# Performance work log

Hardware: AMD Instinct MI355X
Metric: run time of the kernel (lower is better)

## Reference

```python
import jax, jax.numpy as jnp
import numpy as np


def setup_inputs() -> dict:
    key = jax.random.key(0)
    k_user, k_music, k_label, k_mem, k_w = jax.random.split(key, 5)
    B, H, N = 65536, 1024, 256  # batch, hidden (=2*hidden_size), memory slots
    user = jax.random.normal(k_user, (B, H), dtype=jnp.float32)
    music = jax.random.normal(k_music, (B, H), dtype=jnp.float32)
    memory = jax.random.normal(k_mem, (N, H), dtype=jnp.float32) * (1.0 / np.sqrt(H).astype(np.float32))
    W_out = jax.random.normal(k_w, (H, 2), dtype=jnp.float32) * (1.0 / np.sqrt(H).astype(np.float32))
    b_out = jnp.zeros((2,), dtype=jnp.float32)
    label = jax.random.randint(k_label, (B,), 0, 2, dtype=jnp.int64 if jax.config.jax_enable_x64 else jnp.int32)
    return {"user": user, "music": music, "memory": memory, "W_out": W_out, "b_out": b_out, "label": label}


def reference(user, music, memory, W_out, b_out, label):
    # s = user * music  (elementwise interaction)  [B, H]
    s = user * music
    # classification head: Linear(hidden, 2)
    out_result = s @ W_out + b_out  # [B, 2]
    # memory read: softmax(s @ memory^T) @ memory
    attn = jax.nn.softmax(s @ memory.T, axis=1)  # [B, N]
    rel = attn @ memory  # [B, H]
    # translational score: ||user + rel - music||_2 per row
    diff = user + rel - music
    score = jnp.sqrt(jnp.sum(diff * diff, axis=1))  # [B]
    mask = (2 * label - 1).astype(score.dtype)  # {-1, +1}
    loss = jnp.mean(mask * score)
    return loss, out_result
```

## Files before the change

### kernel.cpp

```cpp
#include <hip/hip_runtime.h>
#include <hip/hip_bf16.h>

typedef float ff4 __attribute__((ext_vector_type(4)));
typedef short s8v __attribute__((ext_vector_type(8)));
typedef unsigned int u4v __attribute__((ext_vector_type(4)));
typedef unsigned int u2v __attribute__((ext_vector_type(2)));

#define Hd 1024
#define Nn 256
#define RB 16
#define HSTR 520

__device__ __forceinline__ unsigned bf16r(float f) {
    unsigned u = __builtin_bit_cast(unsigned, f);
    return (u + 0x7FFFu + ((u >> 16) & 1u)) >> 16;
}

__device__ __forceinline__ unsigned cvtpk(float lo, float hi) {
    unsigned r;
    asm("v_cvt_pk_bf16_f32 %0, %1, %2" : "=v"(r) : "v"(lo), "v"(hi));
    return r;
}

__global__ void conv_mem_kernel(const float* __restrict__ mem, unsigned short* __restrict__ memB) {
    int g = blockIdx.x * 256 + threadIdx.x;
    int b = g & 3;
    int r = (g >> 2) & 255;
    int c = g >> 10;
    const float* src = mem + (size_t)r * Hd + c * 32 + b * 8;
    ff4 a0 = *(const ff4*)src;
    ff4 a1 = *(const ff4*)(src + 4);
    u4v v;
    v[0] = bf16r(a0[0]) | (bf16r(a0[1]) << 16);
    v[1] = bf16r(a0[2]) | (bf16r(a0[3]) << 16);
    v[2] = bf16r(a1[0]) | (bf16r(a1[1]) << 16);
    v[3] = bf16r(a1[2]) | (bf16r(a1[3]) << 16);
    *(u4v*)(memB + (size_t)c * 8192 + (size_t)r * 32 + b * 8) = v;
}

__global__ void conv_w_kernel(const float* __restrict__ Wout, unsigned short* __restrict__ Wbf) {
    int t = threadIdx.x;
    int c = t >> 7;
    int h0 = (t & 127) * 8;
    u4v v;
#pragma unroll
    for (int j = 0; j < 4; ++j) {
        unsigned lo = bf16r(Wout[(h0 + 2 * j) * 2 + c]);
        unsigned hi = bf16r(Wout[(h0 + 2 * j + 1) * 2 + c]);
        v[j] = lo | (hi << 16);
    }
    *(u4v*)(Wbf + (size_t)c * Hd + h0) = v;
}

__global__ __launch_bounds__(256) void gram_kernel(const float* __restrict__ mem,
                                                   unsigned short* __restrict__ Gcm) {
    __shared__ float LA[32][132];
    __shared__ float LB[32][132];
    const int t = threadIdx.x;
    const int bi = blockIdx.x >> 3, bj = blockIdx.x & 7;
    const int j = t & 31, i0 = t >> 5;
    float acc0 = 0.f, acc1 = 0.f, acc2 = 0.f, acc3 = 0.f;
    for (int kc = 0; kc < Hd; kc += 128) {
        __syncthreads();
#pragma unroll
        for (int q = 0; q < 4; ++q) {
            int c = t + q * 256;
            int r = c >> 5, fc = (c & 31) << 2;
            *(ff4*)&LA[r][fc] = *(const ff4*)(mem + (size_t)(bi * 32 + r) * Hd + kc + fc);
            *(ff4*)&LB[r][fc] = *(const ff4*)(mem + (size_t)(bj * 32 + r) * Hd + kc + fc);
        }
        __syncthreads();
#pragma unroll 4
        for (int kk = 0; kk < 128; kk += 4) {
            ff4 b = *(const ff4*)&LB[j][kk];
            ff4 a0 = *(const ff4*)&LA[i0][kk];
            ff4 a1 = *(const ff4*)&LA[i0 + 8][kk];
            ff4 a2 = *(const ff4*)&LA[i0 + 16][kk];
            ff4 a3 = *(const ff4*)&LA[i0 + 24][kk];
            acc0 += a0[0]*b[0] + a0[1]*b[1] + a0[2]*b[2] + a0[3]*b[3];
            acc1 += a1[0]*b[0] + a1[1]*b[1] + a1[2]*b[2] + a1[3]*b[3];
            acc2 += a2[0]*b[0] + a2[1]*b[1] + a2[2]*b[2] + a2[3]*b[3];
            acc3 += a3[0]*b[0] + a3[1]*b[1] + a3[2]*b[2] + a3[3]*b[3];
        }
    }
    const size_t base = (size_t)bj * 8192 + (size_t)j;
    Gcm[base + (size_t)(bi * 32 + i0 +  0) * 32] = (unsigned short)bf16r(acc0);
    Gcm[base + (size_t)(bi * 32 + i0 +  8) * 32] = (unsigned short)bf16r(acc1);
    Gcm[base + (size_t)(bi * 32 + i0 + 16) * 32] = (unsigned short)bf16r(acc2);
    Gcm[base + (size_t)(bi * 32 + i0 + 24) * 32] = (unsigned short)bf16r(acc3);
}

__global__ __launch_bounds__(256, 3) void fused_kernel(
    const float* __restrict__ user, const float* __restrict__ music,
    const float* __restrict__ bout, const int* __restrict__ label,
    const unsigned short* __restrict__ memB,
    const unsigned short* __restrict__ Wbf,
    const unsigned short* __restrict__ Gcm,
    float* __restrict__ out, float* __restrict__ partials)
{
    __shared__ __align__(16) unsigned short sS[RB * HSTR];
    __shared__ __align__(16) unsigned short sD[RB * HSTR];
    __shared__ float fMax[64], fSum[64], fCross[64], fQuad[64], fAux[16];
    unsigned short* sAttn = sS;

    const int t = threadIdx.x;
    const int w = t >> 6;
    const int l = t & 63;
    const int la = l & 15, lb = l >> 4;
    const int row0 = blockIdx.x * RB;

    const int srow = t >> 4;
    const int scol = t & 15;
    const float* uRow = user  + (size_t)(row0 + srow) * Hd + scol * 4;
    const float* mRow = music + (size_t)(row0 + srow) * Hd + scol * 4;

    const unsigned short* mbase = memB + w * 2048 + la * 32 + lb * 8;
    const unsigned short* wrowB = Wbf + (size_t)(la < 2 ? la : 1) * Hd + lb * 8;
    const unsigned short* gbase = Gcm + w * 2048 + la * 32 + lb * 8;
    const int aoff = la * HSTR + lb * 8;

    ff4 accL[4], accD[4];
#pragma unroll
    for (int i = 0; i < 4; ++i) { accL[i] = (ff4)0.0f; accD[i] = (ff4)0.0f; }
    ff4 accH = (ff4)0.0f;
    float sd2 = 0.f;

#pragma unroll
    for (int hh = 0; hh < 2; ++hh) {
#pragma unroll
        for (int i = 0; i < 8; ++i) {
            const int off = hh * 512 + 64 * i;
            ff4 uv = *(const ff4*)(uRow + off);
            ff4 mv = *(const ff4*)(mRow + off);
            float s0 = uv[0]*mv[0], s1 = uv[1]*mv[1], s2 = uv[2]*mv[2], s3 = uv[3]*mv[3];
            float d0 = uv[0]-mv[0], d1 = uv[1]-mv[1], d2 = uv[2]-mv[2], d3 = uv[3]-mv[3];
            sd2 = fmaf(d0,d0,sd2); sd2 = fmaf(d1,d1,sd2);
            sd2 = fmaf(d2,d2,sd2); sd2 = fmaf(d3,d3,sd2);
            u2v vs, vd;
            vs[0] = cvtpk(s0, s1); vs[1] = cvtpk(s2, s3);
            vd[0] = cvtpk(d0, d1); vd[1] = cvtpk(d2, d3);
            *(u2v*)(sS + srow * HSTR + scol * 4 + 64 * i) = vs;
            *(u2v*)(sD + srow * HSTR + scol * 4 + 64 * i) = vd;
        }
        __syncthreads();

        {
            const int c0 = hh * 16;
            s8v bMa[4], bMb[4], bWa, bWb, aSa, aSb, aDa, aDb;
#pragma unroll
            for (int nt = 0; nt < 4; ++nt)
                bMa[nt] = *(const s8v*)(mbase + (size_t)c0 * 8192 + nt * 512);
            bWa = *(const s8v*)(wrowB + c0 * 32);
            aSa = *(const s8v*)(sS + aoff);
            aDa = *(const s8v*)(sD + aoff);
#pragma unroll
            for (int kk = 0; kk < 16; kk += 2) {
                const int k1 = (kk + 1) & 15;
#pragma unroll
                for (int nt = 0; nt < 4; ++nt)
                    bMb[nt] = *(const s8v*)(mbase + (size_t)(c0 + k1) * 8192 + nt * 512);
                bWb = *(const s8v*)(wrowB + (c0 + k1) * 32);
                aSb = *(const s8v*)(sS + aoff + k1 * 32);
                aDb = *(const s8v*)(sD + aoff + k1 * 32);
#pragma unroll
                for (int nt = 0; nt < 4; ++nt) {
                    accL[nt] = __builtin_amdgcn_mfma_f32_16x16x32_bf16(aSa, bMa[nt], accL[nt], 0, 0, 0);
                    accD[nt] = __builtin_amdgcn_mfma_f32_16x16x32_bf16(aDa, bMa[nt], accD[nt], 0, 0, 0);
                }
                accH = __builtin_amdgcn_mfma_f32_16x16x32_bf16(aSa, bWa, accH, 0, 0, 0);
                const int k2 = (kk + 2) & 15;
#pragma unroll
                for (int nt = 0; nt < 4; ++nt)
                    bMa[nt] = *(const s8v*)(mbase + (size_t)(c0 + k2) * 8192 + nt * 512);
                bWa = *(const s8v*)(wrowB + (c0 + k2) * 32);
                aSa = *(const s8v*)(sS + aoff + k2 * 32);
                aDa = *(const s8v*)(sD + aoff + k2 * 32);
#pragma unroll
                for (int nt = 0; nt < 4; ++nt) {
                    accL[nt] = __builtin_amdgcn_mfma_f32_16x16x32_bf16(aSb, bMb[nt], accL[nt], 0, 0, 0);
                    accD[nt] = __builtin_amdgcn_mfma_f32_16x16x32_bf16(aDb, bMb[nt], accD[nt], 0, 0, 0);
                }
                accH = __builtin_amdgcn_mfma_f32_16x16x32_bf16(aSb, bWb, accH, 0, 0, 0);
            }
        }
        __syncthreads();
    }

    if (w == 0 && la < 2) {
#pragma unroll
        for (int j = 0; j < 4; ++j) {
            int gr = row0 + lb * 4 + j;
            out[1 + gr * 2 + la] = accH[j] + bout[la];
        }
    }

    sd2 += __shfl_xor(sd2, 1);
    sd2 += __shfl_xor(sd2, 2);
    sd2 += __shfl_xor(sd2, 4);
    sd2 += __shfl_xor(sd2, 8);
    if ((l & 15) == 0) fAux[w * 4 + (l >> 4)] = sd2;

    ff4 mx = accL[0];
#pragma unroll
    for (int nt = 1; nt < 4; ++nt) {
        mx[0] = fmaxf(mx[0], accL[nt][0]); mx[1] = fmaxf(mx[1], accL[nt][1]);
        mx[2] = fmaxf(mx[2], accL[nt][2]); mx[3] = fmaxf(mx[3], accL[nt][3]);
    }
#pragma unroll
    for (int s = 1; s < 16; s <<= 1) {
        mx[0] = fmaxf(mx[0], __shfl_xor(mx[0], s));
        mx[1] = fmaxf(mx[1], __shfl_xor(mx[1], s));
        mx[2] = fmaxf(mx[2], __shfl_xor(mx[2], s));
        mx[3] = fmaxf(mx[3], __shfl_xor(mx[3], s));
    }
    ff4 sm = (ff4)0.0f;
#pragma unroll
    for (int nt = 0; nt < 4; ++nt) {
        sm[0] += __expf(accL[nt][0] - mx[0]); sm[1] += __expf(accL[nt][1] - mx[1]);
        sm[2] += __expf(accL[nt][2] - mx[2]); sm[3] += __expf(accL[nt][3] - mx[3]);
    }
#pragma unroll
    for (int s = 1; s < 16; s <<= 1) {
        sm[0] += __shfl_xor(sm[0], s); sm[1] += __shfl_xor(sm[1], s);
        sm[2] += __shfl_xor(sm[2], s); sm[3] += __shfl_xor(sm[3], s);
    }
    if (la < 4) {
        const int r = lb * 4 + la;
        float mv = (la == 0) ? mx[0] : (la == 1) ? mx[1] : (la == 2) ? mx[2] : mx[3];
        float sv = (la == 0) ? sm[0] : (la == 1) ? sm[1] : (la == 2) ? sm[2] : sm[3];
        fMax[w * 16 + r] = mv;
        fSum[w * 16 + r] = sv;
    }
    __syncthreads();

    ff4 Mr, Dinv;
#pragma unroll
    for (int j = 0; j < 4; ++j) {
        const int r = lb * 4 + j;
        float m0 = fMax[r], m1 = fMax[16 + r], m2 = fMax[32 + r], m3 = fMax[48 + r];
        float M = fmaxf(fmaxf(m0, m1), fmaxf(m2, m3));
        float den = fSum[r] * __expf(m0 - M) + fSum[16 + r] * __expf(m1 - M)
                  + fSum[32 + r] * __expf(m2 - M) + fSum[48 + r] * __expf(m3 - M);
        Mr[j] = M; Dinv[j] = 1.0f / den;
    }
    ff4 cross = (ff4)0.0f;
#pragma unroll
    for (int nt = 0; nt < 4; ++nt) {
        accL[nt][0] = __expf(accL[nt][0] - Mr[0]) * Dinv[0];
        accL[nt][1] = __expf(accL[nt][1] - Mr[1]) * Dinv[1];
        accL[nt][2] = __expf(accL[nt][2] - Mr[2]) * Dinv[2];
        accL[nt][3] = __expf(accL[nt][3] - Mr[3]) * Dinv[3];
        cross[0] = fmaf(accL[nt][0], accD[nt][0], cross[0]);
        cross[1] = fmaf(accL[nt][1], accD[nt][1], cross[1]);
        cross[2] = fmaf(accL[nt][2], accD[nt][2], cross[2]);
        cross[3] = fmaf(accL[nt][3], accD[nt][3], cross[3]);
    }
#pragma unroll
    for (int s = 1; s < 16; s <<= 1) {
        cross[0] += __shfl_xor(cross[0], s); cross[1] += __shfl_xor(cross[1], s);
        cross[2] += __shfl_xor(cross[2], s); cross[3] += __shfl_xor(cross[3], s);
    }
    if (la < 4) {
        const int r = lb * 4 + la;
        float cv = (la == 0) ? cross[0] : (la == 1) ? cross[1] : (la == 2) ? cross[2] : cross[3];
        fCross[w * 16 + r] = cv;
    }
    {
        const int rb = lb << 2;
#pragma unroll
        for (int nt = 0; nt < 4; ++nt) {
            const int cc = w * 64 + nt * 16 + la;
            sAttn[(rb + 0) * 264 + cc] = (unsigned short)bf16r(accL[nt][0]);
            sAttn[(rb + 1) * 264 + cc] = (unsigned short)bf16r(accL[nt][1]);
            sAttn[(rb + 2) * 264 + cc] = (unsigned short)bf16r(accL[nt][2]);
            sAttn[(rb + 3) * 264 + cc] = (unsigned short)bf16r(accL[nt][3]);
        }
    }
    __syncthreads();

    ff4 accG[4];
#pragma unroll
    for (int i = 0; i < 4; ++i) accG[i] = (ff4)0.0f;
#pragma unroll
    for (int ks = 0; ks < 8; ++ks) {
        s8v aA = *(const s8v*)(sAttn + la * 264 + ks * 32 + lb * 8);
        const unsigned short* gp = gbase + (size_t)ks * 8192;
#pragma unroll
        for (int nt = 0; nt < 4; ++nt) {
            s8v bG = *(const s8v*)(gp + nt * 512);
            accG[nt] = __builtin_amdgcn_mfma_f32_16x16x32_bf16(aA, bG, accG[nt], 0, 0, 0);
        }
    }
    ff4 quad = (ff4)0.0f;
#pragma unroll
    for (int nt = 0; nt < 4; ++nt) {
        quad[0] = fmaf(accL[nt][0], accG[nt][0], quad[0]);
        quad[1] = fmaf(accL[nt][1], accG[nt][1], quad[1]);
        quad[2] = fmaf(accL[nt][2], accG[nt][2], quad[2]);
        quad[3] = fmaf(accL[nt][3], accG[nt][3], quad[3]);
    }
#pragma unroll
    for (int s = 1; s < 16; s <<= 1) {
        quad[0] += __shfl_xor(quad[0], s); quad[1] += __shfl_xor(quad[1], s);
        quad[2] += __shfl_xor(quad[2], s); quad[3] += __shfl_xor(quad[3], s);
    }
    if (la < 4) {
        const int r = lb * 4 + la;
        float qv = (la == 0) ? quad[0] : (la == 1) ? quad[1] : (la == 2) ? quad[2] : quad[3];
        fQuad[w * 16 + r] = qv;
    }
    __syncthreads();

    float val = 0.f;
    if (w == 0 && l < 16) {
        float cr  = fCross[l] + fCross[16 + l] + fCross[32 + l] + fCross[48 + l];
        float qd  = fQuad[l] + fQuad[16 + l] + fQuad[32 + l] + fQuad[48 + l];
        float s2 = fAux[l] + 2.0f * cr + qd;
        float sc = sqrtf(fmaxf(s2, 0.0f));
        val = (float)(2 * label[row0 + l] - 1) * sc;
    }
#pragma unroll
    for (int s = 1; s < 64; s <<= 1) val += __shfl_xor(val, s);
    if (t == 0) partials[blockIdx.x] = val;
}

__global__ void finalize_kernel(const float* __restrict__ partials, float* __restrict__ out,
                                int np, float invB) {
    const int t = threadIdx.x;
    float v = 0.f;
    for (int i = t; i < np; i += 256) v += partials[i];
#pragma unroll
    for (int s = 1; s < 64; s <<= 1) v += __shfl_xor(v, s);
    __shared__ float ws4[4];
    if ((t & 63) == 0) ws4[t >> 6] = v;
    __syncthreads();
    if (t == 0) out[0] = (ws4[0] + ws4[1] + ws4[2] + ws4[3]) * invB;
}

extern "C" void kernel_launch(void* const* d_in, const int* in_sizes, int n_in,
                              void* d_out, int out_size, void* d_ws, size_t ws_size,
                              hipStream_t stream) {
    const float* user  = (const float*)d_in[0];
    const float* music = (const float*)d_in[1];
    const float* mem   = (const float*)d_in[2];
    const float* Wout  = (const float*)d_in[3];
    const float* bout  = (const float*)d_in[4];
    const int*   label = (const int*)d_in[5];
    const int Bn   = in_sizes[0] / Hd;
    const int nblk = Bn / RB;

    unsigned short* memB = (unsigned short*)d_ws;
    unsigned short* Wbf  = (unsigned short*)((char*)d_ws + 524288);
    unsigned short* Gcm  = (unsigned short*)((char*)d_ws + 524288 + 4096);
    float* partials      = (float*)((char*)d_ws + 524288 + 4096 + 131072);

    conv_mem_kernel<<<128, 256, 0, stream>>>(mem, memB);
    conv_w_kernel<<<1, 256, 0, stream>>>(Wout, Wbf);
    gram_kernel<<<64, 256, 0, stream>>>(mem, Gcm);
    fused_kernel<<<nblk, 256, 0, stream>>>(user, music, bout, label, memB, Wbf, Gcm,
                                           (float*)d_out, partials);
    finalize_kernel<<<1, 256, 0, stream>>>(partials, (float*)d_out, nblk, 1.0f / (float)Bn);
}
```

Measured before the change: 269.3 us.

## Warp-specialize fused kernel into producer and MFMA consumer waves with double-buffered LDS

The block grows to 512 threads. Four producer waves load user and music, form the product and difference, and write them as bf16 into one of two small LDS slots, each holding a 128-column chunk. Four consumer waves run the MFMA logits and head products on the other slot, so global loads overlap with matrix work. This replaces the earlier two-phase fill-then-compute loop but adds eight barrier rounds and a larger block, which may cost occupancy and add synchronization overhead.

```diff
diff --git a/kernel.cpp b/kernel.cpp
--- a/kernel.cpp
+++ b/kernel.cpp
@@ -9,7 +9,8 @@
 #define Hd 1024
 #define Nn 256
 #define RB 16
-#define HSTR 520
+#define QSTR 136
+#define QSLOT 2176
 
 __device__ __forceinline__ unsigned bf16r(float f) {
     unsigned u = __builtin_bit_cast(unsigned, f);
@@ -90,7 +91,7 @@
     Gcm[base + (size_t)(bi * 32 + i0 + 24) * 32] = (unsigned short)bf16r(acc3);
 }
 
-__global__ __launch_bounds__(256, 3) void fused_kernel(
+__global__ __launch_bounds__(512, 4) void fused_kernel(
     const float* __restrict__ user, const float* __restrict__ music,
     const float* __restrict__ bout, const int* __restrict__ label,
     const unsigned short* __restrict__ memB,
@@ -98,8 +99,8 @@
     const unsigned short* __restrict__ Gcm,
     float* __restrict__ out, float* __restrict__ partials)
 {
-    __shared__ __align__(16) unsigned short sS[RB * HSTR];
-    __shared__ __align__(16) unsigned short sD[RB * HSTR];
+    __shared__ __align__(16) unsigned short sS[2 * QSLOT];
+    __shared__ __align__(16) unsigned short sD[2 * QSLOT];
     __shared__ float fMax[64], fSum[64], fCross[64], fQuad[64], fAux[16];
     unsigned short* sAttn = sS;
 
@@ -108,164 +109,152 @@
     const int l = t & 63;
     const int la = l & 15, lb = l >> 4;
     const int row0 = blockIdx.x * RB;
-
-    const int srow = t >> 4;
-    const int scol = t & 15;
-    const float* uRow = user  + (size_t)(row0 + srow) * Hd + scol * 4;
-    const float* mRow = music + (size_t)(row0 + srow) * Hd + scol * 4;
+    const bool isProd = (w >= 4);
+
+    const int pw = w - 4;
+    const int prow = pw * 4 + (l >> 4);
+    const int pcol = (l & 15) * 4;
+    const float* uP = user  + (size_t)(row0 + prow) * Hd + pcol;
+    const float* mP = music + (size_t)(row0 + prow) * Hd + pcol;
+    float sd2 = 0.f;
 
     const unsigned short* mbase = memB + w * 2048 + la * 32 + lb * 8;
     const unsigned short* wrowB = Wbf + (size_t)(la < 2 ? la : 1) * Hd + lb * 8;
     const unsigned short* gbase = Gcm + w * 2048 + la * 32 + lb * 8;
-    const int aoff = la * HSTR + lb * 8;
 
     ff4 accL[4], accD[4];
 #pragma unroll
     for (int i = 0; i < 4; ++i) { accL[i] = (ff4)0.0f; accD[i] = (ff4)0.0f; }
     ff4 accH = (ff4)0.0f;
-    float sd2 = 0.f;
-
-#pragma unroll
-    for (int hh = 0; hh < 2; ++hh) {
-#pragma unroll
-        for (int i = 0; i < 8; ++i) {
-            const int off = hh * 512 + 64 * i;
-            ff4 uv = *(const ff4*)(uRow + off);
-            ff4 mv = *(const ff4*)(mRow + off);
-            float s0 = uv[0]*mv[0], s1 = uv[1]*mv[1], s2 = uv[2]*mv[2], s3 = uv[3]*mv[3];
-            float d0 = uv[0]-mv[0], d1 = uv[1]-mv[1], d2 = uv[2]-mv[2], d3 = uv[3]-mv[3];
-            sd2 = fmaf(d0,d0,sd2); sd2 = fmaf(d1,d1,sd2);
-            sd2 = fmaf(d2,d2,sd2); sd2 = fmaf(d3,d3,sd2);
-            u2v vs, vd;
-            vs[0] = cvtpk(s0, s1); vs[1] = cvtpk(s2, s3);
-            vd[0] = cvtpk(d0, d1); vd[1] = cvtpk(d2, d3);
-            *(u2v*)(sS + srow * HSTR + scol * 4 + 64 * i) = vs;
-            *(u2v*)(sD + srow * HSTR + scol * 4 + 64 * i) = vd;
+
+#define FILL(QQ, SLOT)                                                          \
+    {                                                                           \
+        _Pragma("unroll")                                                       \
+        for (int i = 0; i < 2; ++i) {                                           \
+            const int off = (QQ) * 128 + i * 64;                                \
+            ff4 uv = *(const ff4*)(uP + off);                                   \
+            ff4 mv = *(const ff4*)(mP + off);                                   \
+            float s0 = uv[0]*mv[0], s1 = uv[1]*mv[1], s2 = uv[2]*mv[2], s3 = uv[3]*mv[3]; \
+            float d0 = uv[0]-mv[0], d1 = uv[1]-mv[1], d2 = uv[2]-mv[2], d3 = uv[3]-mv[3]; \
+            sd2 = fmaf(d0,d0,sd2); sd2 = fmaf(d1,d1,sd2);                       \
+            sd2 = fmaf(d2,d2,sd2); sd2 = fmaf(d3,d3,sd2);                       \
+            u2v vs, vd;                                                         \
+            vs[0] = cvtpk(s0, s1); vs[1] = cvtpk(s2, s3);                       \
+            vd[0] = cvtpk(d0, d1); vd[1] = cvtpk(d2, d3);                       \
+            *(u2v*)(sS + (SLOT) * QSLOT + prow * QSTR + i * 64 + pcol) = vs;    \
+            *(u2v*)(sD + (SLOT) * QSLOT + prow * QSTR + i * 64 + pcol) = vd;    \
+        }                                                                       \
+    }
+
+    if (isProd) FILL(0, 0)
+    __syncthreads();
+
+    for (int q = 0; q < 8; ++q) {
+        if (isProd) {
+            if (q < 7) FILL(q + 1, (q + 1) & 1)
+        } else {
+            const int s = q & 1;
+#pragma unroll
+            for (int kk = 0; kk < 4; ++kk) {
+                const int c = q * 4 + kk;
+                const unsigned short* mp = mbase + (size_t)c * 8192;
+                s8v aS = *(const s8v*)(sS + s * QSLOT + la * QSTR + kk * 32 + lb * 8);
+                s8v aD = *(const s8v*)(sD + s * QSLOT + la * QSTR + kk * 32 + lb * 8);
+                s8v bW = *(const s8v*)(wrowB + c * 32);
+#pragma unroll
+                for (int nt = 0; nt < 4; ++nt) {
+                    s8v bM = *(const s8v*)(mp + nt * 512);
+                    accL[nt] = __builtin_amdgcn_mfma_f32_16x16x32_bf16(aS, bM, accL[nt], 0, 0, 0);
+                    accD[nt] = __builtin_amdgcn_mfma_f32_16x16x32_bf16(aD, bM, accD[nt], 0, 0, 0);
+                }
+                accH = __builtin_amdgcn_mfma_f32_16x16x32_bf16(aS, bW, accH, 0, 0, 0);
+            }
         }
         __syncthreads();
-
-        {
-            const int c0 = hh * 16;
-            s8v bMa[4], bMb[4], bWa, bWb, aSa, aSb, aDa, aDb;
-#pragma unroll
-            for (int nt = 0; nt < 4; ++nt)
-                bMa[nt] = *(const s8v*)(mbase + (size_t)c0 * 8192 + nt * 512);
-            bWa = *(const s8v*)(wrowB + c0 * 32);
-            aSa = *(const s8v*)(sS + aoff);
-            aDa = *(const s8v*)(sD + aoff);
-#pragma unroll
-            for (int kk = 0; kk < 16; kk += 2) {
-                const int k1 = (kk + 1) & 15;
-#pragma unroll
-                for (int nt = 0; nt < 4; ++nt)
-                    bMb[nt] = *(const s8v*)(mbase + (size_t)(c0 + k1) * 8192 + nt * 512);
-                bWb = *(const s8v*)(wrowB + (c0 + k1) * 32);
-                aSb = *(const s8v*)(sS + aoff + k1 * 32);
-                aDb = *(const s8v*)(sD + aoff + k1 * 32);
-#pragma unroll
-                for (int nt = 0; nt < 4; ++nt) {
-                    accL[nt] = __builtin_amdgcn_mfma_f32_16x16x32_bf16(aSa, bMa[nt], accL[nt], 0, 0, 0);
-                    accD[nt] = __builtin_amdgcn_mfma_f32_16x16x32_bf16(aDa, bMa[nt], accD[nt], 0, 0, 0);
-                }
-                accH = __builtin_amdgcn_mfma_f32_16x16x32_bf16(aSa, bWa, accH, 0, 0, 0);
-                const int k2 = (kk + 2) & 15;
-#pragma unroll
-                for (int nt = 0; nt < 4; ++nt)
-                    bMa[nt] = *(const s8v*)(mbase + (size_t)(c0 + k2) * 8192 + nt * 512);
-                bWa = *(const s8v*)(wrowB + (c0 + k2) * 32);
-                aSa = *(const s8v*)(sS + aoff + k2 * 32);
-                aDa = *(const s8v*)(sD + aoff + k2 * 32);
-#pragma unroll
-                for (int nt = 0; nt < 4; ++nt) {
-                    accL[nt] = __builtin_amdgcn_mfma_f32_16x16x32_bf16(aSb, bMb[nt], accL[nt], 0, 0, 0);
-                    accD[nt] = __builtin_amdgcn_mfma_f32_16x16x32_bf16(aDb, bMb[nt], accD[nt], 0, 0, 0);
-                }
-                accH = __builtin_amdgcn_mfma_f32_16x16x32_bf16(aSb, bWb, accH, 0, 0, 0);
+    }
+#undef FILL
+
+    if (isProd) {
+        sd2 += __shfl_xor(sd2, 1);
+        sd2 += __shfl_xor(sd2, 2);
+        sd2 += __shfl_xor(sd2, 4);
+        sd2 += __shfl_xor(sd2, 8);
+        if ((l & 15) == 0) fAux[prow] = sd2;
+    }
+    if (!isProd) {
+        if (w == 0 && la < 2) {
+#pragma unroll
+            for (int j = 0; j < 4; ++j) {
+                int gr = row0 + lb * 4 + j;
+                out[1 + gr * 2 + la] = accH[j] + bout[la];
             }
         }
-        __syncthreads();
-    }
-
-    if (w == 0 && la < 2) {
+        ff4 mx = accL[0];
+#pragma unroll
+        for (int nt = 1; nt < 4; ++nt) {
+            mx[0] = fmaxf(mx[0], accL[nt][0]); mx[1] = fmaxf(mx[1], accL[nt][1]);
+            mx[2] = fmaxf(mx[2], accL[nt][2]); mx[3] = fmaxf(mx[3], accL[nt][3]);
+        }
+#pragma unroll
+        for (int s = 1; s < 16; s <<= 1) {
+            mx[0] = fmaxf(mx[0], __shfl_xor(mx[0], s));
+            mx[1] = fmaxf(mx[1], __shfl_xor(mx[1], s));
+            mx[2] = fmaxf(mx[2], __shfl_xor(mx[2], s));
+            mx[3] = fmaxf(mx[3], __shfl_xor(mx[3], s));
+        }
+        ff4 sm = (ff4)0.0f;
+#pragma unroll
+        for (int nt = 0; nt < 4; ++nt) {
+            sm[0] += __expf(accL[nt][0] - mx[0]); sm[1] += __expf(accL[nt][1] - mx[1]);
+            sm[2] += __expf(accL[nt][2] - mx[2]); sm[3] += __expf(accL[nt][3] - mx[3]);
+        }
+#pragma unroll
+        for (int s = 1; s < 16; s <<= 1) {
+            sm[0] += __shfl_xor(sm[0], s); sm[1] += __shfl_xor(sm[1], s);
+            sm[2] += __shfl_xor(sm[2], s); sm[3] += __shfl_xor(sm[3], s);
+        }
+        if (la < 4) {
+            const int r = lb * 4 + la;
+            float mv = (la == 0) ? mx[0] : (la == 1) ? mx[1] : (la == 2) ? mx[2] : mx[3];
+            float sv = (la == 0) ? sm[0] : (la == 1) ? sm[1] : (la == 2) ? sm[2] : sm[3];
+            fMax[w * 16 + r] = mv;
+            fSum[w * 16 + r] = sv;
+        }
+    }
+    __syncthreads();
+
+    ff4 Mr, Dinv, cross = (ff4)0.0f;
+    if (!isProd) {
 #pragma unroll
         for (int j = 0; j < 4; ++j) {
-            int gr = row0 + lb * 4 + j;
-            out[1 + gr * 2 + la] = accH[j] + bout[la];
-        }
-    }
-
-    sd2 += __shfl_xor(sd2, 1);
-    sd2 += __shfl_xor(sd2, 2);
-    sd2 += __shfl_xor(sd2, 4);
-    sd2 += __shfl_xor(sd2, 8);
-    if ((l & 15) == 0) fAux[w * 4 + (l >> 4)] = sd2;
-
-    ff4 mx = accL[0];
-#pragma unroll
-    for (int nt = 1; nt < 4; ++nt) {
-        mx[0] = fmaxf(mx[0], accL[nt][0]); mx[1] = fmaxf(mx[1], accL[nt][1]);
-        mx[2] = fmaxf(mx[2], accL[nt][2]); mx[3] = fmaxf(mx[3], accL[nt][3]);
-    }
-#pragma unroll
-    for (int s = 1; s < 16; s <<= 1) {
-        mx[0] = fmaxf(mx[0], __shfl_xor(mx[0], s));
-        mx[1] = fmaxf(mx[1], __shfl_xor(mx[1], s));
-        mx[2] = fmaxf(mx[2], __shfl_xor(mx[2], s));
-        mx[3] = fmaxf(mx[3], __shfl_xor(mx[3], s));
-    }
-    ff4 sm = (ff4)0.0f;
-#pragma unroll
-    for (int nt = 0; nt < 4; ++nt) {
-        sm[0] += __expf(accL[nt][0] - mx[0]); sm[1] += __expf(accL[nt][1] - mx[1]);
-        sm[2] += __expf(accL[nt][2] - mx[2]); sm[3] += __expf(accL[nt][3] - mx[3]);
-    }
-#pragma unroll
-    for (int s = 1; s < 16; s <<= 1) {
-        sm[0] += __shfl_xor(sm[0], s); sm[1] += __shfl_xor(sm[1], s);
-        sm[2] += __shfl_xor(sm[2], s); sm[3] += __shfl_xor(sm[3], s);
-    }
-    if (la < 4) {
-        const int r = lb * 4 + la;
-        float mv = (la == 0) ? mx[0] : (la == 1) ? mx[1] : (la == 2) ? mx[2] : mx[3];
-        float sv = (la == 0) ? sm[0] : (la == 1) ? sm[1] : (la == 2) ? sm[2] : sm[3];
-        fMax[w * 16 + r] = mv;
-        fSum[w * 16 + r] = sv;
-    }
-    __syncthreads();
-
-    ff4 Mr, Dinv;
-#pragma unroll
-    for (int j = 0; j < 4; ++j) {
-        const int r = lb * 4 + j;
-        float m0 = fMax[r], m1 = fMax[16 + r], m2 = fMax[32 + r], m3 = fMax[48 + r];
-        float M = fmaxf(fmaxf(m0, m1), fmaxf(m2, m3));
-        float den = fSum[r] * __expf(m0 - M) + fSum[16 + r] * __expf(m1 - M)
-                  + fSum[32 + r] * __expf(m2 - M) + fSum[48 + r] * __expf(m3 - M);
-        Mr[j] = M; Dinv[j] = 1.0f / den;
-    }
-    ff4 cross = (ff4)0.0f;
-#pragma unroll
-    for (int nt = 0; nt < 4; ++nt) {
-        accL[nt][0] = __expf(accL[nt][0] - Mr[0]) * Dinv[0];
-        accL[nt][1] = __expf(accL[nt][1] - Mr[1]) * Dinv[1];
-        accL[nt][2] = __expf(accL[nt][2] - Mr[2]) * Dinv[2];
-        accL[nt][3] = __expf(accL[nt][3] - Mr[3]) * Dinv[3];
-        cross[0] = fmaf(accL[nt][0], accD[nt][0], cross[0]);
-        cross[1] = fmaf(accL[nt][1], accD[nt][1], cross[1]);
-        cross[2] = fmaf(accL[nt][2], accD[nt][2], cross[2]);
-        cross[3] = fmaf(accL[nt][3], accD[nt][3], cross[3]);
-    }
-#pragma unroll
-    for (int s = 1; s < 16; s <<= 1) {
-        cross[0] += __shfl_xor(cross[0], s); cross[1] += __shfl_xor(cross[1], s);
-        cross[2] += __shfl_xor(cross[2], s); cross[3] += __shfl_xor(cross[3], s);
-    }
-    if (la < 4) {
-        const int r = lb * 4 + la;
-        float cv = (la == 0) ? cross[0] : (la == 1) ? cross[1] : (la == 2) ? cross[2] : cross[3];
-        fCross[w * 16 + r] = cv;
-    }
-    {
+            const int r = lb * 4 + j;
+            float m0 = fMax[r], m1 = fMax[16 + r], m2 = fMax[32 + r], m3 = fMax[48 + r];
+            float M = fmaxf(fmaxf(m0, m1), fmaxf(m2, m3));
+            float den = fSum[r] * __expf(m0 - M) + fSum[16 + r] * __expf(m1 - M)
+                      + fSum[32 + r] * __expf(m2 - M) + fSum[48 + r] * __expf(m3 - M);
+            Mr[j] = M; Dinv[j] = 1.0f / den;
+        }
+#pragma unroll
+        for (int nt = 0; nt < 4; ++nt) {
+            accL[nt][0] = __expf(accL[nt][0] - Mr[0]) * Dinv[0];
+            accL[nt][1] = __expf(accL[nt][1] - Mr[1]) * Dinv[1];
+            accL[nt][2] = __expf(accL[nt][2] - Mr[2]) * Dinv[2];
+            accL[nt][3] = __expf(accL[nt][3] - Mr[3]) * Dinv[3];
+            cross[0] = fmaf(accL[nt][0], accD[nt][0], cross[0]);
+            cross[1] = fmaf(accL[nt][1], accD[nt][1], cross[1]);
+            cross[2] = fmaf(accL[nt][2], accD[nt][2], cross[2]);
+            cross[3] = fmaf(accL[nt][3], accD[nt][3], cross[3]);
+        }
+#pragma unroll
+        for (int s = 1; s < 16; s <<= 1) {
+            cross[0] += __shfl_xor(cross[0], s); cross[1] += __shfl_xor(cross[1], s);
+            cross[2] += __shfl_xor(cross[2], s); cross[3] += __shfl_xor(cross[3], s);
+        }
+        if (la < 4) {
+            const int r = lb * 4 + la;
+            float cv = (la == 0) ? cross[0] : (la == 1) ? cross[1] : (la == 2) ? cross[2] : cross[3];
+            fCross[w * 16 + r] = cv;
+        }
         const int rb = lb << 2;
 #pragma unroll
         for (int nt = 0; nt < 4; ++nt) {
@@ -278,36 +267,38 @@
     }
     __syncthreads();
 
-    ff4 accG[4];
-#pragma unroll
-    for (int i = 0; i < 4; ++i) accG[i] = (ff4)0.0f;
-#pragma unroll
-    for (int ks = 0; ks < 8; ++ks) {
-        s8v aA = *(const s8v*)(sAttn + la * 264 + ks * 32 + lb * 8);
-        const unsigned short* gp = gbase + (size_t)ks * 8192;
+    if (!isProd) {
+        ff4 accG[4];
+#pragma unroll
+        for (int i = 0; i < 4; ++i) accG[i] = (ff4)0.0f;
+#pragma unroll
+        for (int ks = 0; ks < 8; ++ks) {
+            s8v aA = *(const s8v*)(sAttn + la * 264 + ks * 32 + lb * 8);
+            const unsigned short* gp = gbase + (size_t)ks * 8192;
+#pragma unroll
+            for (int nt = 0; nt < 4; ++nt) {
+                s8v bG = *(const s8v*)(gp + nt * 512);
+                accG[nt] = __builtin_amdgcn_mfma_f32_16x16x32_bf16(aA, bG, accG[nt], 0, 0, 0);
+            }
+        }
+        ff4 quad = (ff4)0.0f;
 #pragma unroll
         for (int nt = 0; nt < 4; ++nt) {
-            s8v bG = *(const s8v*)(gp + nt * 512);
-            accG[nt] = __builtin_amdgcn_mfma_f32_16x16x32_bf16(aA, bG, accG[nt], 0, 0, 0);
-        }
-    }
-    ff4 quad = (ff4)0.0f;
-#pragma unroll
-    for (int nt = 0; nt < 4; ++nt) {
-        quad[0] = fmaf(accL[nt][0], accG[nt][0], quad[0]);
-        quad[1] = fmaf(accL[nt][1], accG[nt][1], quad[1]);
-        quad[2] = fmaf(accL[nt][2], accG[nt][2], quad[2]);
-        quad[3] = fmaf(accL[nt][3], accG[nt][3], quad[3]);
-    }
-#pragma unroll
-    for (int s = 1; s < 16; s <<= 1) {
-        quad[0] += __shfl_xor(quad[0], s); quad[1] += __shfl_xor(quad[1], s);
-        quad[2] += __shfl_xor(quad[2], s); quad[3] += __shfl_xor(quad[3], s);
-    }
-    if (la < 4) {
-        const int r = lb * 4 + la;
-        float qv = (la == 0) ? quad[0] : (la == 1) ? quad[1] : (la == 2) ? quad[2] : quad[3];
-        fQuad[w * 16 + r] = qv;
+            quad[0] = fmaf(accL[nt][0], accG[nt][0], quad[0]);
+            quad[1] = fmaf(accL[nt][1], accG[nt][1], quad[1]);
+            quad[2] = fmaf(accL[nt][2], accG[nt][2], quad[2]);
+            quad[3] = fmaf(accL[nt][3], accG[nt][3], quad[3]);
+        }
+#pragma unroll
+        for (int s = 1; s < 16; s <<= 1) {
+            quad[0] += __shfl_xor(quad[0], s); quad[1] += __shfl_xor(quad[1], s);
+            quad[2] += __shfl_xor(quad[2], s); quad[3] += __shfl_xor(quad[3], s);
+        }
+        if (la < 4) {
+            const int r = lb * 4 + la;
+            float qv = (la == 0) ? quad[0] : (la == 1) ? quad[1] : (la == 2) ? quad[2] : quad[3];
+            fQuad[w * 16 + r] = qv;
+        }
     }
     __syncthreads();
 
@@ -319,9 +310,11 @@
         float sc = sqrtf(fmaxf(s2, 0.0f));
         val = (float)(2 * label[row0 + l] - 1) * sc;
     }
-#pragma unroll
-    for (int s = 1; s < 64; s <<= 1) val += __shfl_xor(val, s);
-    if (t == 0) partials[blockIdx.x] = val;
+    if (w == 0) {
+#pragma unroll
+        for (int s = 1; s < 64; s <<= 1) val += __shfl_xor(val, s);
+        if (l == 0) partials[blockIdx.x] = val;
+    }
 }
 
 __global__ void finalize_kernel(const float* __restrict__ partials, float* __restrict__ out,
@@ -357,7 +350,7 @@
     conv_mem_kernel<<<128, 256, 0, stream>>>(mem, memB);
     conv_w_kernel<<<1, 256, 0, stream>>>(Wout, Wbf);
     gram_kernel<<<64, 256, 0, stream>>>(mem, Gcm);
-    fused_kernel<<<nblk, 256, 0, stream>>>(user, music, bout, label, memB, Wbf, Gcm,
+    fused_kernel<<<nblk, 512, 0, stream>>>(user, music, bout, label, memB, Wbf, Gcm,
                                            (float*)d_out, partials);
     finalize_kernel<<<1, 256, 0, stream>>>(partials, (float*)d_out, nblk, 1.0f / (float)Bn);
 }
```

Measured after the change: 415.5 us. 1.54x slower.
